# Optimization experiments

Measured on AMD Instinct MI355X. Metric: run time of the kernel, lower is better.

## Reference

```python
import jax, jax.numpy as jnp
import numpy as np

EPS = 1e-5

def _conv1x1(x, w, b):
    # x: [B,C,...], w: [O,C], b: [O]
    y = jnp.einsum('oc,bc...->bo...', w, x)
    return y + b.reshape((1, -1) + (1,) * (x.ndim - 2))

def _bn(x, g, be, m, v):
    # inference-mode BatchNorm with running stats (PyTorch eps=1e-5)
    s = (1, -1) + (1,) * (x.ndim - 2)
    return (x - m.reshape(s)) * (g.reshape(s) / jnp.sqrt(v.reshape(s) + EPS)) + be.reshape(s)

def _patches3x3(x):
    # F.unfold(kernel=3, pad=1, stride=1, dil=1): [B,C,H,W] -> [B,C,9,H,W], row-major kernel order
    B, C, H, W = x.shape
    xp = jnp.pad(x, ((0, 0), (0, 0), (1, 1), (1, 1)))
    return jnp.stack([xp[:, :, ky:ky + H, kx:kx + W] for ky in range(3) for kx in range(3)], axis=2)

def setup_inputs() -> dict:
    key = jax.random.key(0)
    ks = jax.random.split(key, 40)
    B, Cin, H, W = 4, 16, 192, 192
    Cm = 64  # mlp[-1]
    d = {}
    d['x'] = jax.random.normal(ks[0], (B, Cin, H, W), jnp.float32)
    d['group_mask'] = jnp.ones((B, 1, H, W), jnp.float32)
    d['group_xyz'] = jax.random.normal(ks[1], (B, 3, 9, H, W), jnp.float32)
    def bnp(k, c):
        k1, k2, k3, k4 = jax.random.split(k, 4)
        return (1.0 + 0.1 * jax.random.normal(k1, (c,)), 0.1 * jax.random.normal(k2, (c,)),
                0.1 * jax.random.normal(k3, (c,)), 0.5 + jax.random.uniform(k4, (c,)))
    d['w0'] = 0.1 * jax.random.normal(ks[2], (Cm, Cin)); d['b0'] = 0.01 * jax.random.normal(ks[3], (Cm,))
    d['g0'], d['beta0'], d['m0'], d['v0'] = bnp(ks[4], Cm)
    wn_dims = [(8, 3), (8, 8), (16, 8)]
    for i, (o, c) in enumerate(wn_dims):
        d[f'wn_w{i}'] = 0.3 * jax.random.normal(ks[5 + 3 * i], (o, c))
        d[f'wn_b{i}'] = 0.01 * jax.random.normal(ks[6 + 3 * i], (o,))
        d[f'wn_g{i}'], d[f'wn_beta{i}'], d[f'wn_m{i}'], d[f'wn_v{i}'] = bnp(ks[7 + 3 * i], o)
    d['lw'] = 0.05 * jax.random.normal(ks[20], (Cm, 16 * Cm)); d['lb'] = 0.01 * jax.random.normal(ks[21], (Cm,))
    d['lg'], d['lbeta'], d['lm'], d['lv'] = bnp(ks[22], Cm)
    return d

def reference(x, group_mask, group_xyz,
              w0, b0, g0, beta0, m0, v0,
              wn_w0, wn_b0, wn_g0, wn_beta0, wn_m0, wn_v0,
              wn_w1, wn_b1, wn_g1, wn_beta1, wn_m1, wn_v1,
              wn_w2, wn_b2, wn_g2, wn_beta2, wn_m2, wn_v2,
              lw, lb, lg, lbeta, lm, lv):
    # mlp_convs chain (single layer here)
    x = jax.nn.relu(_bn(_conv1x1(x, w0, b0), g0, beta0, m0, v0))  # [B,Cm,H,W]
    B, _, N, H, W = group_xyz.shape
    # WeightNet on local coords: [B,3,N,H*W] -> [B,16,N,H*W]
    gz = group_xyz.reshape(B, 3, N, H * W)
    for w, b, g, be, m, v in ((wn_w0, wn_b0, wn_g0, wn_beta0, wn_m0, wn_v0),
                              (wn_w1, wn_b1, wn_g1, wn_beta1, wn_m1, wn_v1),
                              (wn_w2, wn_b2, wn_g2, wn_beta2, wn_m2, wn_v2)):
        gz = jax.nn.relu(_bn(_conv1x1(gz, w, b), g, be, m, v))
    gz = gz.reshape(B, 16, N, H, W)
    p = _patches3x3(x)  # [B,Cm,9,H,W]
    C = p.shape[1]
    # per-pixel matmul: [B,H,W,C,9] @ [B,H,W,9,16] -> [B,H,W,C,16]
    out = jnp.einsum('bckhw,bokhw->bhwco', p, gz)
    out = out.reshape(B, H, W, C * 16).transpose(0, 3, 1, 2)  # [B,16*Cm,H,W]
    return jax.nn.relu(_bn(_conv1x1(out, lw, lb), lg, lbeta, lm, lv))
```

## Files before the change

kernel.cpp:

```cpp
#include <hip/hip_runtime.h>
#include <hip/hip_bf16.h>

#define HH 192
#define WW 192
#define HWPROD (192*192)
#define EPSBN 1e-5f

typedef _Float16 f16x8 __attribute__((ext_vector_type(8)));
typedef _Float16 f16x4 __attribute__((ext_vector_type(4)));
typedef float f32x4 __attribute__((ext_vector_type(4)));

__global__ void prep_k(const float* __restrict__ w0, const float* __restrict__ b0,
                       const float* __restrict__ g0, const float* __restrict__ beta0,
                       const float* __restrict__ m0, const float* __restrict__ v0,
                       const float* __restrict__ wnw0, const float* __restrict__ wnb0,
                       const float* __restrict__ wng0, const float* __restrict__ wnbe0,
                       const float* __restrict__ wnm0, const float* __restrict__ wnv0,
                       const float* __restrict__ wnw1, const float* __restrict__ wnb1,
                       const float* __restrict__ wng1, const float* __restrict__ wnbe1,
                       const float* __restrict__ wnm1, const float* __restrict__ wnv1,
                       const float* __restrict__ wnw2, const float* __restrict__ wnb2,
                       const float* __restrict__ wng2, const float* __restrict__ wnbe2,
                       const float* __restrict__ wnm2, const float* __restrict__ wnv2,
                       const float* __restrict__ lw, const float* __restrict__ lb,
                       const float* __restrict__ lg, const float* __restrict__ lbeta,
                       const float* __restrict__ lm, const float* __restrict__ lv,
                       _Float16* __restrict__ whF,
                       float* __restrict__ lbf,
                       float* __restrict__ w0f, float* __restrict__ b0f,
                       float* __restrict__ wnP)
{
    int idx = blockIdx.x * 256 + threadIdx.x;
    if (idx < 65536) {
        int j    = idx & 7;
        int lane = (idx >> 3) & 63;
        int kg   = (idx >> 9) & 31;
        int nt   = idx >> 14;
        int k = kg * 32 + ((lane >> 4) & 3) * 8 + j;
        int n = nt * 16 + (lane & 15);
        float s = lg[n] * rsqrtf(lv[n] + EPSBN);
        whF[idx] = (_Float16)(lw[n * 1024 + k] * s);
    } else if (idx < 65600) {
        int j = idx - 65536;
        float s = lg[j] * rsqrtf(lv[j] + EPSBN);
        lbf[j] = (lb[j] - lm[j]) * s + lbeta[j];
    } else if (idx < 66624) {
        int t = idx - 65600;
        int o = t >> 4;
        float s = g0[o] * rsqrtf(v0[o] + EPSBN);
        w0f[t] = w0[t] * s;
    } else if (idx < 66688) {
        int o = idx - 66624;
        float s = g0[o] * rsqrtf(v0[o] + EPSBN);
        b0f[o] = (b0[o] - m0[o]) * s + beta0[o];
    } else if (idx < 66936) {
        int t = idx - 66688;
        if (t < 24)       { int o = t / 3;           float s = wng0[o] * rsqrtf(wnv0[o] + EPSBN); wnP[t] = wnw0[t] * s; }
        else if (t < 32)  { int o = t - 24;          float s = wng0[o] * rsqrtf(wnv0[o] + EPSBN); wnP[t] = (wnb0[o] - wnm0[o]) * s + wnbe0[o]; }
        else if (t < 96)  { int t2 = t - 32;  int o = t2 >> 3; float s = wng1[o] * rsqrtf(wnv1[o] + EPSBN); wnP[t] = wnw1[t2] * s; }
        else if (t < 104) { int o = t - 96;          float s = wng1[o] * rsqrtf(wnv1[o] + EPSBN); wnP[t] = (wnb1[o] - wnm1[o]) * s + wnbe1[o]; }
        else if (t < 232) { int t2 = t - 104; int o = t2 >> 3; float s = wng2[o] * rsqrtf(wnv2[o] + EPSBN); wnP[t] = wnw2[t2] * s; }
        else              { int o = t - 232;         float s = wng2[o] * rsqrtf(wnv2[o] + EPSBN); wnP[t] = (wnb2[o] - wnm2[o]) * s + wnbe2[o]; }
    }
}

__global__ __launch_bounds__(256) void conv0_k(const float* __restrict__ x,
                                               const float* __restrict__ w0f,
                                               const float* __restrict__ b0f,
                                               _Float16* __restrict__ x1L)
{
    const int pix = blockIdx.x * 256 + threadIdx.x;
    const int b = pix / HWPROD;
    const int p = pix - b * HWPROD;

    float xv[16];
#pragma unroll
    for (int cin = 0; cin < 16; cin++)
        xv[cin] = x[((size_t)b * 16 + cin) * HWPROD + p];

    _Float16* outp = x1L + (size_t)pix * 64;
#pragma unroll
    for (int co = 0; co < 64; co += 4) {
        f32x4 a = { b0f[co], b0f[co + 1], b0f[co + 2], b0f[co + 3] };
#pragma unroll
        for (int cin = 0; cin < 16; cin++) {
            float xc = xv[cin];
            a.x += w0f[(co + 0) * 16 + cin] * xc;
            a.y += w0f[(co + 1) * 16 + cin] * xc;
            a.z += w0f[(co + 2) * 16 + cin] * xc;
            a.w += w0f[(co + 3) * 16 + cin] * xc;
        }
        a.x = fmaxf(a.x, 0.f); a.y = fmaxf(a.y, 0.f);
        a.z = fmaxf(a.z, 0.f); a.w = fmaxf(a.w, 0.f);
        *(f16x4*)(outp + co) = __builtin_convertvector(a, f16x4);
    }
}

__global__ __launch_bounds__(512, 4) void pconv_main_k(const float* __restrict__ gxyz,
                                                       const _Float16* __restrict__ x1L,
                                                       const _Float16* __restrict__ whF,
                                                       const float* __restrict__ lbf,
                                                       const float* __restrict__ wnP,
                                                       float* __restrict__ out)
{
    __shared__ __align__(16) char smem[64608];
    _Float16* xt  = reinterpret_cast<_Float16*>(smem);
    _Float16* gzF = reinterpret_cast<_Float16*>(smem + 28512);
    _Float16* A0  = reinterpret_cast<_Float16*>(smem + 28512);
    _Float16* A1  = reinterpret_cast<_Float16*>(smem + 47968);
    float*    Cb  = reinterpret_cast<float*>(smem);

    const int tid = threadIdx.x;
    const int bid = blockIdx.x;
    const int b   = bid / (HH * 3);
    const int rem = bid % (HH * 3);
    const int h   = rem / 3;
    const int wc0 = (rem % 3) * 64;

    for (int q = tid; q < 1584; q += 512) {
        int c8   = q & 7;
        int colr = q >> 3;
        int col  = colr % 66;
        int r    = colr / 66;
        int hr = h + r - 1;
        int wc = wc0 + col - 1;
        f16x8 v = {};
        if (hr >= 0 && hr < HH && wc >= 0 && wc < WW) {
            v = *(const f16x8*)(x1L + (((size_t)b * HH + hr) * WW + wc) * 64 + c8 * 8);
        }
        *(f16x8*)&xt[(r * 66 + col) * 72 + c8 * 8] = v;
    }

    for (int u = tid; u < 576; u += 512) {
        int pixu = u & 63, tap = u >> 6;
        size_t base = ((size_t)(b * 3) * 9 + tap) * HWPROD + (size_t)h * WW + wc0 + pixu;
        float z0 = gxyz[base];
        float z1 = gxyz[base + (size_t)9 * HWPROD];
        float z2 = gxyz[base + (size_t)18 * HWPROD];
        float h0[8], h1[8];
#pragma unroll
        for (int o = 0; o < 8; o++) {
            float a = wnP[24 + o] + wnP[o * 3 + 0] * z0 + wnP[o * 3 + 1] * z1 + wnP[o * 3 + 2] * z2;
            h0[o] = fmaxf(a, 0.f);
        }
#pragma unroll
        for (int o = 0; o < 8; o++) {
            float a = wnP[96 + o];
#pragma unroll
            for (int c = 0; c < 8; c++) a += wnP[32 + o * 8 + c] * h0[c];
            h1[o] = fmaxf(a, 0.f);
        }
        float g[16];
#pragma unroll
        for (int o = 0; o < 16; o++) {
            float a = wnP[232 + o];
#pragma unroll
            for (int c = 0; c < 8; c++) a += wnP[104 + o * 8 + c] * h1[c];
            g[o] = fmaxf(a, 0.f);
        }
        f16x8 lo, hi;
#pragma unroll
        for (int o = 0; o < 8; o++) { lo[o] = (_Float16)g[o]; hi[o] = (_Float16)g[o + 8]; }
        *(f16x8*)&gzF[pixu * 152 + tap * 16]     = lo;
        *(f16x8*)&gzF[pixu * 152 + tap * 16 + 8] = hi;
    }
    __syncthreads();

    const int pix = tid & 63;
    const int oq  = (tid >> 6) & 3;
    const int cH  = tid >> 8;
    const int lane = tid & 63;
    const int wv   = tid >> 6;
    const int nt   = wv & 3;
    const int mt2  = wv >> 2;

    f32x4 gq[9];
#pragma unroll
    for (int t = 0; t < 9; t++)
        gq[t] = __builtin_convertvector(*(const f16x4*)&gzF[pix * 152 + t * 16 + oq * 4], f32x4);
    __syncthreads();

    const int mt  = pix >> 4;
    const int lf0 = (pix & 15) + 16 * (oq >> 1);
    const int jb  = (oq & 1) * 4;

    auto phase1 = [&](int cc, _Float16* Ab) {
        f32x4 av[4];
#pragma unroll
        for (int c = 0; c < 4; c++) av[c] = f32x4{0.f, 0.f, 0.f, 0.f};
#pragma unroll
        for (int ky = 0; ky < 3; ky++) {
#pragma unroll
            for (int kx = 0; kx < 3; kx++) {
                f16x4 xq = *(const f16x4*)&xt[(ky * 66 + pix + kx) * 72 + cc * 8 + cH * 4];
                f32x4 xf = __builtin_convertvector(xq, f32x4);
                f32x4 g  = gq[ky * 3 + kx];
#pragma unroll
                for (int c = 0; c < 4; c++) {
                    f32x4 xb = { xf[c], xf[c], xf[c], xf[c] };
                    av[c] = __builtin_elementwise_fma(xb, g, av[c]);
                }
            }
        }
#pragma unroll
        for (int c = 0; c < 4; c++) {
            const int c8 = cH * 4 + c;
            const int kb = c8 >> 1;
            const int laneF = lf0 + 32 * (c8 & 1);
            *(f16x4*)&Ab[(kb * 4 + mt) * 520 + laneF * 8 + jb] =
                __builtin_convertvector(av[c], f16x4);
        }
    };

    const f16x8* whF8 = (const f16x8*)whF;
    f32x4 facc[2];
    facc[0] = f32x4{0.f, 0.f, 0.f, 0.f};
    facc[1] = f32x4{0.f, 0.f, 0.f, 0.f};

    phase1(0, A0);
    __syncthreads();

#pragma unroll 2
    for (int cc = 0; cc < 8; cc++) {
        const _Float16* Ac = (cc & 1) ? A1 : A0;
#pragma unroll
        for (int kb = 0; kb < 4; kb++) {
            const int kg = cc * 4 + kb;
            f16x8 a0 = *(const f16x8*)&Ac[(kb * 4 + 2 * mt2) * 520 + lane * 8];
            f16x8 a1 = *(const f16x8*)&Ac[(kb * 4 + 2 * mt2 + 1) * 520 + lane * 8];
            f16x8 wh = whF8[((nt * 32 + kg) << 6) + lane];
            facc[0] = __builtin_amdgcn_mfma_f32_16x16x32_f16(a0, wh, facc[0], 0, 0, 0);
            facc[1] = __builtin_amdgcn_mfma_f32_16x16x32_f16(a1, wh, facc[1], 0, 0, 0);
        }
        if (cc < 7) phase1(cc + 1, (cc & 1) ? A0 : A1);
        __syncthreads();
    }

    {
        const int n = nt * 16 + (lane & 15);
        const float bias = lbf[n];
#pragma unroll
        for (int m = 0; m < 2; m++) {
            const int pixm = (2 * mt2 + m) * 16 + (lane >> 4) * 4;
#pragma unroll
            for (int r = 0; r < 4; r++)
                Cb[n * 67 + pixm + r] = fmaxf(facc[m][r] + bias, 0.f);
        }
    }
    __syncthreads();
    {
        const int pixq = tid & 63, jq = tid >> 6;
        size_t ob = ((size_t)b * 64 + jq * 8) * HWPROD + (size_t)h * WW + wc0 + pixq;
#pragma unroll
        for (int i = 0; i < 8; i++) {
            out[ob + (size_t)i * HWPROD] = Cb[(jq * 8 + i) * 67 + pixq];
        }
    }
}

extern "C" void kernel_launch(void* const* d_in, const int* in_sizes, int n_in,
                              void* d_out, int out_size, void* d_ws, size_t ws_size,
                              hipStream_t stream) {
    const float* x    = (const float*)d_in[0];
    const float* gxyz = (const float*)d_in[2];

    char* ws = (char*)d_ws;
    _Float16* x1L = (_Float16*)ws;
    _Float16* whF = x1L + 9437184;
    float* lbf = (float*)(whF + 65536);
    float* w0f = lbf + 64;
    float* b0f = w0f + 1024;
    float* wnP = b0f + 64;

    prep_k<<<262, 256, 0, stream>>>(
        (const float*)d_in[3],  (const float*)d_in[4],  (const float*)d_in[5],
        (const float*)d_in[6],  (const float*)d_in[7],  (const float*)d_in[8],
        (const float*)d_in[9],  (const float*)d_in[10], (const float*)d_in[11],
        (const float*)d_in[12], (const float*)d_in[13], (const float*)d_in[14],
        (const float*)d_in[15], (const float*)d_in[16], (const float*)d_in[17],
        (const float*)d_in[18], (const float*)d_in[19], (const float*)d_in[20],
        (const float*)d_in[21], (const float*)d_in[22], (const float*)d_in[23],
        (const float*)d_in[24], (const float*)d_in[25], (const float*)d_in[26],
        (const float*)d_in[27], (const float*)d_in[28], (const float*)d_in[29],
        (const float*)d_in[30], (const float*)d_in[31], (const float*)d_in[32],
        whF, lbf, w0f, b0f, wnP);

    conv0_k<<<576, 256, 0, stream>>>(x, w0f, b0f, x1L);

    pconv_main_k<<<4 * HH * 3, 512, 0, stream>>>(gxyz, x1L, whF, lbf, wnP,
                                                 (float*)d_out);
}
```

Before: 251.0 us.

## Reorder K dimension to output-major and compute per-pixel patch matmul in packed fp16

Reorders the K index of the final 1x1 conv weights so each phase handles two weightnet outputs across all 64 channels instead of channel groups. Stores the weightnet result transposed as fp16 pairs in LDS, and computes the per-pixel 9-tap product with packed fp16 FMAs on 8 channels at once instead of fp32 FMAs with broadcast. The intent is to cut phase1 ALU work and register use. The cost is more LDS (78 KB vs 64 KB), which may lower occupancy, and fp16 accumulation over 9 taps, which loses precision.

```diff
diff --git a/kernel.cpp b/kernel.cpp
--- a/kernel.cpp
+++ b/kernel.cpp
@@ -8,6 +8,7 @@
 
 typedef _Float16 f16x8 __attribute__((ext_vector_type(8)));
 typedef _Float16 f16x4 __attribute__((ext_vector_type(4)));
+typedef _Float16 f16x2 __attribute__((ext_vector_type(2)));
 typedef float f32x4 __attribute__((ext_vector_type(4)));
 
 __global__ void prep_k(const float* __restrict__ w0, const float* __restrict__ b0,
@@ -37,9 +38,10 @@
         int kg   = (idx >> 9) & 31;
         int nt   = idx >> 14;
         int k = kg * 32 + ((lane >> 4) & 3) * 8 + j;
+        int o = k >> 6, c = k & 63;
         int n = nt * 16 + (lane & 15);
         float s = lg[n] * rsqrtf(lv[n] + EPSBN);
-        whF[idx] = (_Float16)(lw[n * 1024 + k] * s);
+        whF[idx] = (_Float16)(lw[n * 1024 + c * 16 + o] * s);
     } else if (idx < 65600) {
         int j = idx - 65536;
         float s = lg[j] * rsqrtf(lv[j] + EPSBN);
@@ -103,11 +105,11 @@
                                                        const float* __restrict__ wnP,
                                                        float* __restrict__ out)
 {
-    __shared__ __align__(16) char smem[64608];
+    __shared__ __align__(16) char smem[78640];
     _Float16* xt  = reinterpret_cast<_Float16*>(smem);
-    _Float16* gzF = reinterpret_cast<_Float16*>(smem + 28512);
-    _Float16* A0  = reinterpret_cast<_Float16*>(smem + 28512);
-    _Float16* A1  = reinterpret_cast<_Float16*>(smem + 47968);
+    f16x2*    gzT = reinterpret_cast<f16x2*>(smem + 26928);
+    _Float16* A0  = reinterpret_cast<_Float16*>(smem + 45360);
+    _Float16* A1  = reinterpret_cast<_Float16*>(smem + 62000);
     float*    Cb  = reinterpret_cast<float*>(smem);
 
     const int tid = threadIdx.x;
@@ -128,7 +130,7 @@
         if (hr >= 0 && hr < HH && wc >= 0 && wc < WW) {
             v = *(const f16x8*)(x1L + (((size_t)b * HH + hr) * WW + wc) * 64 + c8 * 8);
         }
-        *(f16x8*)&xt[(r * 66 + col) * 72 + c8 * 8] = v;
+        *(f16x8*)&xt[(r * 66 + col) * 68 + c8 * 8] = v;
     }
 
     for (int u = tid; u < 576; u += 512) {
@@ -158,58 +160,41 @@
             for (int c = 0; c < 8; c++) a += wnP[104 + o * 8 + c] * h1[c];
             g[o] = fmaxf(a, 0.f);
         }
-        f16x8 lo, hi;
-#pragma unroll
-        for (int o = 0; o < 8; o++) { lo[o] = (_Float16)g[o]; hi[o] = (_Float16)g[o + 8]; }
-        *(f16x8*)&gzF[pixu * 152 + tap * 16]     = lo;
-        *(f16x8*)&gzF[pixu * 152 + tap * 16 + 8] = hi;
+#pragma unroll
+        for (int op = 0; op < 8; op++) {
+            gzT[(tap * 8 + op) * 64 + pixu] = f16x2{(_Float16)g[2 * op], (_Float16)g[2 * op + 1]};
+        }
     }
     __syncthreads();
 
     const int pix = tid & 63;
-    const int oq  = (tid >> 6) & 3;
-    const int cH  = tid >> 8;
+    const int c8  = tid >> 6;
     const int lane = tid & 63;
     const int wv   = tid >> 6;
     const int nt   = wv & 3;
     const int mt2  = wv >> 2;
 
-    f32x4 gq[9];
-#pragma unroll
-    for (int t = 0; t < 9; t++)
-        gq[t] = __builtin_convertvector(*(const f16x4*)&gzF[pix * 152 + t * 16 + oq * 4], f32x4);
-    __syncthreads();
-
-    const int mt  = pix >> 4;
-    const int lf0 = (pix & 15) + 16 * (oq >> 1);
-    const int jb  = (oq & 1) * 4;
+    const int mt    = pix >> 4;
+    const int laneF = (pix & 15) + 16 * (c8 & 3);
+    const int kgl   = c8 >> 2;
 
     auto phase1 = [&](int cc, _Float16* Ab) {
-        f32x4 av[4];
-#pragma unroll
-        for (int c = 0; c < 4; c++) av[c] = f32x4{0.f, 0.f, 0.f, 0.f};
+        f16x8 av0 = {}, av1 = {};
 #pragma unroll
         for (int ky = 0; ky < 3; ky++) {
 #pragma unroll
             for (int kx = 0; kx < 3; kx++) {
-                f16x4 xq = *(const f16x4*)&xt[(ky * 66 + pix + kx) * 72 + cc * 8 + cH * 4];
-                f32x4 xf = __builtin_convertvector(xq, f32x4);
-                f32x4 g  = gq[ky * 3 + kx];
-#pragma unroll
-                for (int c = 0; c < 4; c++) {
-                    f32x4 xb = { xf[c], xf[c], xf[c], xf[c] };
-                    av[c] = __builtin_elementwise_fma(xb, g, av[c]);
-                }
+                const int t = ky * 3 + kx;
+                f16x8 xq = *(const f16x8*)&xt[(ky * 66 + pix + kx) * 68 + c8 * 8];
+                f16x2 g2 = gzT[(t * 8 + cc) * 64 + pix];
+                f16x8 s0 = __builtin_shufflevector(g2, g2, 0, 0, 0, 0, 0, 0, 0, 0);
+                f16x8 s1 = __builtin_shufflevector(g2, g2, 1, 1, 1, 1, 1, 1, 1, 1);
+                av0 = __builtin_elementwise_fma(xq, s0, av0);
+                av1 = __builtin_elementwise_fma(xq, s1, av1);
             }
         }
-#pragma unroll
-        for (int c = 0; c < 4; c++) {
-            const int c8 = cH * 4 + c;
-            const int kb = c8 >> 1;
-            const int laneF = lf0 + 32 * (c8 & 1);
-            *(f16x4*)&Ab[(kb * 4 + mt) * 520 + laneF * 8 + jb] =
-                __builtin_convertvector(av[c], f16x4);
-        }
+        *(f16x8*)&Ab[((0 + kgl) * 4 + mt) * 520 + laneF * 8] = av0;
+        *(f16x8*)&Ab[((2 + kgl) * 4 + mt) * 520 + laneF * 8] = av1;
     };
 
     const f16x8* whF8 = (const f16x8*)whF;
```

After: 334.5 us. 1.33x slower.
